# Performance work log

Measured on AMD Instinct MI355X. Metric: run time of the kernel, lower is better.

## Reference

```python
import jax, jax.numpy as jnp
import numpy as np

NBIT = 4          # weight bit-width
GROUP_SIZE = 128  # weight quantization group size (divides k)
HAS_WEIGHT_ZEROS = True


def _quant_dequant_weights(w, group_size=GROUP_SIZE, nbit=NBIT, has_zeros=HAS_WEIGHT_ZEROS):
    # Mirrors torchao _quantize + quantize_per_channel_group, then dequantizes
    # (the native kernel dequantizes inline with the matmul; math is identical).
    qmin = -(1 << (nbit - 1))
    qmax = (1 << (nbit - 1)) - 1
    n, k = w.shape
    g = w.reshape(-1, group_size)                      # [n*k/gs, gs]
    vmin = g.min(axis=1, keepdims=True)
    vmax = g.max(axis=1, keepdims=True)
    scales = (vmax - vmin) / (qmax - qmin)             # per-group scale
    if has_zeros:
        zeros = qmin - jnp.round(vmin / scales)
    else:
        zeros = jnp.zeros_like(scales)
    q = jnp.clip(jnp.round(g / scales) + zeros, qmin, qmax)
    deq = (q - zeros) * scales
    return deq.reshape(n, k)


def _dyn_quant_dequant_act(x):
    # Dynamic per-token (per-row) asymmetric int8 activation quantization.
    qmin, qmax = -128, 127
    xmin = x.min(axis=-1, keepdims=True)
    xmax = x.max(axis=-1, keepdims=True)
    scale = (xmax - xmin) / (qmax - qmin)
    zero = qmin - jnp.round(xmin / scale)
    q = jnp.clip(jnp.round(x / scale) + zero, qmin, qmax)
    return (q - zero) * scale


def setup_inputs() -> dict:
    key = jax.random.key(0)
    k1, k2 = jax.random.split(key)
    x = jax.random.normal(k1, (4, 2048, 4096), dtype=jnp.float32)
    weights = jax.random.normal(k2, (4096, 4096), dtype=jnp.float32) * 0.02
    return {"x": x, "weights": weights}


def reference(x, weights):
    w_deq = _quant_dequant_weights(weights)            # [n, k]
    x_deq = _dyn_quant_dequant_act(x)                  # [..., m, k]
    # y[..., m, n] = x_deq @ w_deq^T
    return jnp.einsum('bmk,nk->bmn', x_deq, w_deq)
```

## Files before the change

### kernel.cpp

```cpp
#include <hip/hip_runtime.h>
#include <hip/hip_bf16.h>
#include <cfloat>

typedef __attribute__((ext_vector_type(8))) short bf16x8;
typedef __attribute__((ext_vector_type(4))) float f32x4;

#define M_DIM 8192
#define N_DIM 4096
#define K_DIM 4096

__device__ inline ushort f2bf(float f) {
    unsigned u = __float_as_uint(f);
    unsigned r = (u + 0x7FFFu + ((u >> 16) & 1u)) >> 16;
    return (ushort)r;
}

#define SWZ(x) ((x) ^ ((((x) >> 7) & 7) << 4))

__global__ __launch_bounds__(256) void w_dequant(const float* __restrict__ w,
                                                 ushort* __restrict__ wq) {
    int g = blockIdx.x * 4 + (threadIdx.x >> 6);
    int lane = threadIdx.x & 63;
    const float* src = w + (size_t)g * 128;
    float2 v = *(const float2*)(src + lane * 2);
    float mn = fminf(v.x, v.y), mx = fmaxf(v.x, v.y);
#pragma unroll
    for (int s = 1; s < 64; s <<= 1) {
        mn = fminf(mn, __shfl_xor(mn, s));
        mx = fmaxf(mx, __shfl_xor(mx, s));
    }
    float scale = (mx - mn) / 15.0f;
    float zero  = -8.0f - rintf(mn / scale);
    float q0 = fminf(fmaxf(rintf(v.x / scale) + zero, -8.0f), 7.0f);
    float q1 = fminf(fmaxf(rintf(v.y / scale) + zero, -8.0f), 7.0f);
    ushort2 o;
    o.x = f2bf((q0 - zero) * scale);
    o.y = f2bf((q1 - zero) * scale);
    *(ushort2*)(wq + (size_t)g * 128 + lane * 2) = o;
}

__global__ __launch_bounds__(256) void act_qdq(const float* __restrict__ x,
                                               ushort* __restrict__ xq) {
    __shared__ float smn[4], smx[4];
    int row = blockIdx.x;
    const float* xr = x + (size_t)row * K_DIM;
    ushort* xo = xq + (size_t)row * K_DIM;
    int t = threadIdx.x;
    float4 v[4];
    float mn = FLT_MAX, mx = -FLT_MAX;
#pragma unroll
    for (int i = 0; i < 4; i++) {
        v[i] = ((const float4*)xr)[t + i * 256];
        mn = fminf(mn, fminf(fminf(v[i].x, v[i].y), fminf(v[i].z, v[i].w)));
        mx = fmaxf(mx, fmaxf(fmaxf(v[i].x, v[i].y), fmaxf(v[i].z, v[i].w)));
    }
#pragma unroll
    for (int s = 1; s < 64; s <<= 1) {
        mn = fminf(mn, __shfl_xor(mn, s));
        mx = fmaxf(mx, __shfl_xor(mx, s));
    }
    int w = t >> 6;
    if ((t & 63) == 0) { smn[w] = mn; smx[w] = mx; }
    __syncthreads();
    mn = fminf(fminf(smn[0], smn[1]), fminf(smn[2], smn[3]));
    mx = fmaxf(fmaxf(smx[0], smx[1]), fmaxf(smx[2], smx[3]));
    float scale = (mx - mn) / 255.0f;
    float zero  = -128.0f - rintf(mn / scale);
#pragma unroll
    for (int i = 0; i < 4; i++) {
        ushort4 o;
        float q;
        q = fminf(fmaxf(rintf(v[i].x / scale) + zero, -128.0f), 127.0f); o.x = f2bf((q - zero) * scale);
        q = fminf(fmaxf(rintf(v[i].y / scale) + zero, -128.0f), 127.0f); o.y = f2bf((q - zero) * scale);
        q = fminf(fmaxf(rintf(v[i].z / scale) + zero, -128.0f), 127.0f); o.z = f2bf((q - zero) * scale);
        q = fminf(fmaxf(rintf(v[i].w / scale) + zero, -128.0f), 127.0f); o.w = f2bf((q - zero) * scale);
        ((ushort4*)xo)[t + i * 256] = o;
    }
}

#define BM 256
#define BN 256
#define BK 64
#define NT (K_DIM / BK)

__global__ __launch_bounds__(512, 1) void gemm_bt8(const ushort* __restrict__ A,
                                                   const ushort* __restrict__ B,
                                                   float* __restrict__ C) {
    __shared__ __align__(16) ushort As[2][BM * BK];
    __shared__ __align__(16) ushort Bs[2][BN * BK];

    const int nbx = N_DIM / BN;
    const int nwg = (M_DIM / BM) * nbx;
    int bid = blockIdx.x;
    bid = (bid & 7) * (nwg / 8) + (bid >> 3);
    int mb = bid / nbx, nb = bid % nbx;
    size_t m0 = (size_t)mb * BM, n0 = (size_t)nb * BN;

    const int t = threadIdx.x;
    const int w = t >> 6, lane = t & 63;
    const int wm = w >> 2, wn = w & 3;
    const int lr = lane & 15;
    const int lk = (lane >> 4) << 3;

    const ushort* Ab = A + m0 * K_DIM;
    const ushort* Bb = B + n0 * K_DIM;

    const int mask7 = (lr & 7) << 4;
    const int lp0 = lr * 128 + ((lk * 2) ^ mask7);
    const int lp1 = lr * 128 + ((64 + lk * 2) ^ mask7);
    const char* A_k0 = (const char*)As + wm * 4096 + lp0;
    const char* A_k1 = (const char*)As + wm * 4096 + lp1;
    const char* B_k0 = (const char*)Bs + wn * 8192 + lp0;
    const char* B_k1 = (const char*)Bs + wn * 8192 + lp1;

    int off_q[4], dst_q[4];
#pragma unroll
    for (int rq = 0; rq < 4; rq++) {
        int base = rq * 8192 + w * 1024;
        int lg = SWZ(base + lane * 16);
        off_q[rq] = (lg >> 7) * K_DIM + ((lg & 127) >> 1);
        dst_q[rq] = base;
    }

    auto STAGE = [&](int T, int qq) {
        if (T >= NT) return;
        int d = T & 1;
        bool isA = qq < 4;
        int rq = qq & 3;
        ushort* l = isA ? As[d] : Bs[d];
        const ushort* g = (isA ? Ab : Bb) + (size_t)T * BK + off_q[rq];
        __builtin_amdgcn_global_load_lds(
            (const __attribute__((address_space(1))) unsigned int*)g,
            (__attribute__((address_space(3))) unsigned int*)((char*)l + dst_q[rq]),
            16, 0, 0);
    };

    f32x4 acc[8][4] = {};
    bf16x8 afr[2][2];
    bf16x8 bfr[4][2];

#define LOADA(d, q) do {                                                          \
    _Pragma("unroll") for (int ii = 0; ii < 2; ii++) {                            \
        afr[ii][0] = *(const bf16x8*)(A_k0 + (d) * 32768 + ((q) * 64 + ii * 16) * 128); \
        afr[ii][1] = *(const bf16x8*)(A_k1 + (d) * 32768 + ((q) * 64 + ii * 16) * 128); \
    } } while (0)
#define LOADB(d) do {                                                             \
    _Pragma("unroll") for (int ni = 0; ni < 4; ni++) {                            \
        bfr[ni][0] = *(const bf16x8*)(B_k0 + (d) * 32768 + ni * 2048);            \
        bfr[ni][1] = *(const bf16x8*)(B_k1 + (d) * 32768 + ni * 2048);            \
    } } while (0)

#define PHASE(d, q, sT1, sq1, sT2, sq2, vm) do {                                  \
    if ((q) == 0) LOADB(d);                                                       \
    LOADA(d, q);                                                                  \
    STAGE(sT1, sq1);                                                              \
    STAGE(sT2, sq2);                                                              \
    __builtin_amdgcn_s_barrier();                                                 \
    asm volatile("s_waitcnt lgkmcnt(0)" ::: "memory");                            \
    __builtin_amdgcn_sched_barrier(0);                                            \
    __builtin_amdgcn_s_setprio(1);                                                \
    _Pragma("unroll") for (int kk = 0; kk < 2; kk++)                              \
    _Pragma("unroll") for (int ii = 0; ii < 2; ii++)                              \
    _Pragma("unroll") for (int ni = 0; ni < 4; ni++)                              \
        acc[(q) * 2 + ii][ni] = __builtin_amdgcn_mfma_f32_16x16x32_bf16(          \
            afr[ii][kk], bfr[ni][kk], acc[(q) * 2 + ii][ni], 0, 0, 0);            \
    __builtin_amdgcn_s_setprio(0);                                                \
    if ((vm) == 1) asm volatile("s_waitcnt vmcnt(8)" ::: "memory");               \
    if ((vm) == 2) asm volatile("s_waitcnt vmcnt(0)" ::: "memory");               \
    __builtin_amdgcn_s_barrier();                                                 \
  } while (0)

    STAGE(0, 0); STAGE(0, 1); STAGE(0, 2); STAGE(0, 3);
    STAGE(0, 4); STAGE(0, 5); STAGE(0, 6); STAGE(0, 7);
    STAGE(1, 4); STAGE(1, 5); STAGE(1, 6); STAGE(1, 7);
    STAGE(1, 0); STAGE(1, 1);
    asm volatile("s_waitcnt vmcnt(6)" ::: "memory");
    __builtin_amdgcn_s_barrier();

#pragma unroll 1
    for (int i = 0; i < NT / 2 - 1; i++) {
        int T0 = 2 * i;
        PHASE(0, 0, T0 + 1, 2, T0 + 1, 3, 1);
        PHASE(0, 1, T0 + 2, 4, T0 + 2, 5, 1);
        PHASE(0, 2, T0 + 2, 6, T0 + 2, 7, 1);
        PHASE(0, 3, T0 + 2, 0, T0 + 2, 1, 1);
        PHASE(1, 0, T0 + 2, 2, T0 + 2, 3, 1);
        PHASE(1, 1, T0 + 3, 4, T0 + 3, 5, 1);
        PHASE(1, 2, T0 + 3, 6, T0 + 3, 7, 1);
        PHASE(1, 3, T0 + 3, 0, T0 + 3, 1, 1);
    }

    PHASE(0, 0, NT - 1, 2, NT - 1, 3, 1);
    PHASE(0, 1, NT, 0, NT, 0, 1);
    PHASE(0, 2, NT, 0, NT, 0, 1);
    PHASE(0, 3, NT, 0, NT, 0, 2);
    PHASE(1, 0, NT, 0, NT, 0, 0);
    PHASE(1, 1, NT, 0, NT, 0, 0);
    PHASE(1, 2, NT, 0, NT, 0, 0);
    PHASE(1, 3, NT, 0, NT, 0, 0);
#undef PHASE
#undef LOADA
#undef LOADB

    int fq = lane >> 4;
#pragma unroll
    for (int mi = 0; mi < 8; mi++) {
#pragma unroll
        for (int ni = 0; ni < 4; ni++) {
#pragma unroll
            for (int r = 0; r < 4; r++) {
                size_t crow = m0 + (mi >> 1) * 64 + wm * 32 + (mi & 1) * 16 + fq * 4 + r;
                C[crow * N_DIM + n0 + wn * 64 + ni * 16 + lr] = acc[mi][ni][r];
            }
        }
    }
}

extern "C" void kernel_launch(void* const* d_in, const int* in_sizes, int n_in,
                              void* d_out, int out_size, void* d_ws, size_t ws_size,
                              hipStream_t stream) {
    const float* x = (const float*)d_in[0];
    const float* w = (const float*)d_in[1];
    float* out = (float*)d_out;

    ushort* wq = (ushort*)d_ws;
    ushort* xq = (ushort*)((char*)d_ws + (size_t)N_DIM * K_DIM * 2);

    hipLaunchKernelGGL(w_dequant, dim3((N_DIM * K_DIM / 128) / 4), dim3(256), 0, stream, w, wq);
    hipLaunchKernelGGL(act_qdq, dim3(M_DIM), dim3(256), 0, stream, x, xq);
    hipLaunchKernelGGL(gemm_bt8, dim3((M_DIM / BM) * (N_DIM / BN)), dim3(512), 0, stream, xq, wq, out);
}
```

Baseline: 304.5 us.

## Switch GEMM inner loop to 32x32x16 bf16 MFMA tiles

Replaces the 16x16x32 MFMA tiling with 32x32x16 MFMA instructions. Each wave now computes 4x2 tiles of 32x32 with 16-wide accumulators, and the LDS fragment addressing and output mapping are reworked to match. The larger MFMA halves the number of instructions and raises operand reuse per LDS read, which lowers LDS read traffic. In exchange the row mapping per wave changes (wm*128 blocks) and there is a risk of LDS bank conflicts under the existing swizzle.

Measured after the change: 336.3 us. +10.4%, slower.

```diff
diff --git a/kernel.cpp b/kernel.cpp
--- a/kernel.cpp
+++ b/kernel.cpp
@@ -3,7 +3,7 @@
 #include <cfloat>
 
 typedef __attribute__((ext_vector_type(8))) short bf16x8;
-typedef __attribute__((ext_vector_type(4))) float f32x4;
+typedef __attribute__((ext_vector_type(16))) float f32x16;
 
 #define M_DIM 8192
 #define N_DIM 4096
@@ -99,19 +99,20 @@
     const int t = threadIdx.x;
     const int w = t >> 6, lane = t & 63;
     const int wm = w >> 2, wn = w & 3;
-    const int lr = lane & 15;
-    const int lk = (lane >> 4) << 3;
+    const int l31 = lane & 31;
+    const int lg5 = lane >> 5;
 
     const ushort* Ab = A + m0 * K_DIM;
     const ushort* Bb = B + n0 * K_DIM;
 
-    const int mask7 = (lr & 7) << 4;
-    const int lp0 = lr * 128 + ((lk * 2) ^ mask7);
-    const int lp1 = lr * 128 + ((64 + lk * 2) ^ mask7);
-    const char* A_k0 = (const char*)As + wm * 4096 + lp0;
-    const char* A_k1 = (const char*)As + wm * 4096 + lp1;
-    const char* B_k0 = (const char*)Bs + wn * 8192 + lp0;
-    const char* B_k1 = (const char*)Bs + wn * 8192 + lp1;
+    const int mask7 = (lane & 7) << 4;
+    int a_s[4], b_s[4];
+#pragma unroll
+    for (int s = 0; s < 4; s++) {
+        int col = (s * 32 + lg5 * 16) ^ mask7;
+        a_s[s] = (wm * 128 + l31) * 128 + col;
+        b_s[s] = (wn * 64 + l31) * 128 + col;
+    }
 
     int off_q[4], dst_q[4];
 #pragma unroll
@@ -135,20 +136,19 @@
             16, 0, 0);
     };
 
-    f32x4 acc[8][4] = {};
-    bf16x8 afr[2][2];
-    bf16x8 bfr[4][2];
+    f32x16 acc[4][2] = {};
+    bf16x8 afr[4];
+    bf16x8 bfr[2][4];
 
 #define LOADA(d, q) do {                                                          \
-    _Pragma("unroll") for (int ii = 0; ii < 2; ii++) {                            \
-        afr[ii][0] = *(const bf16x8*)(A_k0 + (d) * 32768 + ((q) * 64 + ii * 16) * 128); \
-        afr[ii][1] = *(const bf16x8*)(A_k1 + (d) * 32768 + ((q) * 64 + ii * 16) * 128); \
-    } } while (0)
+    _Pragma("unroll") for (int s = 0; s < 4; s++)                                 \
+        afr[s] = *(const bf16x8*)((const char*)As + a_s[s] + (d) * 32768 + (q) * 4096); \
+    } while (0)
 #define LOADB(d) do {                                                             \
-    _Pragma("unroll") for (int ni = 0; ni < 4; ni++) {                            \
-        bfr[ni][0] = *(const bf16x8*)(B_k0 + (d) * 32768 + ni * 2048);            \
-        bfr[ni][1] = *(const bf16x8*)(B_k1 + (d) * 32768 + ni * 2048);            \
-    } } while (0)
+    _Pragma("unroll") for (int nt = 0; nt < 2; nt++)                              \
+    _Pragma("unroll") for (int s = 0; s < 4; s++)                                 \
+        bfr[nt][s] = *(const bf16x8*)((const char*)Bs + b_s[s] + (d) * 32768 + nt * 4096); \
+    } while (0)
 
 #define PHASE(d, q, sT1, sq1, sT2, sq2, vm) do {                                  \
     if ((q) == 0) LOADB(d);                                                       \
@@ -159,11 +159,10 @@
     asm volatile("s_waitcnt lgkmcnt(0)" ::: "memory");                            \
     __builtin_amdgcn_sched_barrier(0);                                            \
     __builtin_amdgcn_s_setprio(1);                                                \
-    _Pragma("unroll") for (int kk = 0; kk < 2; kk++)                              \
-    _Pragma("unroll") for (int ii = 0; ii < 2; ii++)                              \
-    _Pragma("unroll") for (int ni = 0; ni < 4; ni++)                              \
-        acc[(q) * 2 + ii][ni] = __builtin_amdgcn_mfma_f32_16x16x32_bf16(          \
-            afr[ii][kk], bfr[ni][kk], acc[(q) * 2 + ii][ni], 0, 0, 0);            \
+    _Pragma("unroll") for (int s = 0; s < 4; s++)                                 \
+    _Pragma("unroll") for (int nt = 0; nt < 2; nt++)                              \
+        acc[q][nt] = __builtin_amdgcn_mfma_f32_32x32x16_bf16(                     \
+            afr[s], bfr[nt][s], acc[q][nt], 0, 0, 0);                             \
     __builtin_amdgcn_s_setprio(0);                                                \
     if ((vm) == 1) asm volatile("s_waitcnt vmcnt(8)" ::: "memory");               \
     if ((vm) == 2) asm volatile("s_waitcnt vmcnt(0)" ::: "memory");               \
@@ -202,15 +201,14 @@
 #undef LOADA
 #undef LOADB
 
-    int fq = lane >> 4;
-#pragma unroll
-    for (int mi = 0; mi < 8; mi++) {
-#pragma unroll
-        for (int ni = 0; ni < 4; ni++) {
-#pragma unroll
-            for (int r = 0; r < 4; r++) {
-                size_t crow = m0 + (mi >> 1) * 64 + wm * 32 + (mi & 1) * 16 + fq * 4 + r;
-                C[crow * N_DIM + n0 + wn * 64 + ni * 16 + lr] = acc[mi][ni][r];
+#pragma unroll
+    for (int q = 0; q < 4; q++) {
+#pragma unroll
+        for (int nt = 0; nt < 2; nt++) {
+#pragma unroll
+            for (int r = 0; r < 16; r++) {
+                size_t crow = m0 + wm * 128 + q * 32 + (r & 3) + 8 * (r >> 2) + 4 * lg5;
+                C[crow * N_DIM + n0 + wn * 64 + nt * 32 + l31] = acc[q][nt][r];
             }
         }
     }
```
